# Kernel tuning notes

Measured on AMD Instinct MI355X. Metric: run time of the kernel, lower is better.

Reference implementation:

```python
import jax, jax.numpy as jnp
import numpy as np


def dct_matrix(n):
    # orthonormal DCT-II matrix, matches scipy.fftpack.dct(norm='ortho')
    k = jnp.arange(n, dtype=jnp.float32)[:, None]
    i = jnp.arange(n, dtype=jnp.float32)[None, :]
    D = jnp.cos(jnp.pi * (2.0 * i + 1.0) * k / (2.0 * n))
    s = jnp.where(k == 0, jnp.sqrt(1.0 / n), jnp.sqrt(2.0 / n))
    return (D * s).astype(jnp.float32)


def mad_mask(h, w):
    eps = 1e-10
    v1 = int(min(h, w) * 0.1)
    v2 = int(min(h, w) * 0.7)
    v3 = min(h, w)
    xy = jnp.maximum(jnp.arange(h, dtype=jnp.float32)[:, None],
                     jnp.arange(w, dtype=jnp.float32)[None, :])
    m = jnp.where(xy <= v1, 1.0 - xy / (v1 + eps) * 0.95,
        jnp.where(xy <= v2, 0.01,
        jnp.where(xy <= v3, (xy - v2) / (v3 - v2) * 0.3, 0.5)))
    return m.astype(jnp.float32)


def setup_inputs() -> dict:
    key = jax.random.key(0)
    ks = jax.random.split(key, 8)
    num_layers, token_length, C = 24, 100, 1024
    N, B = 1024, 32  # h = w = 32
    patch = 16
    val = np.sqrt(6.0 / float(3 * patch * patch + C))
    feats = jax.random.normal(ks[0], (1 + N, B, C), dtype=jnp.float32)
    learnable_tokens = jax.random.uniform(ks[1], (num_layers, token_length, C),
                                          minval=-val, maxval=val, dtype=jnp.float32)
    lim = 1.0 / np.sqrt(C)
    W_t2f = jax.random.uniform(ks[2], (C, C), minval=-lim, maxval=lim, dtype=jnp.float32)
    b_t2f = jax.random.uniform(ks[3], (C,), minval=-lim, maxval=lim, dtype=jnp.float32)
    W_df = jax.random.uniform(ks[4], (C, C), minval=-lim, maxval=lim, dtype=jnp.float32)
    b_df = jax.random.uniform(ks[5], (C,), minval=-lim, maxval=lim, dtype=jnp.float32)
    return {
        'feats': feats,
        'layer': 5,
        'learnable_tokens': learnable_tokens,
        'scale': jnp.float32(0.001),
        'W_t2f': W_t2f,
        'b_t2f': b_t2f,
        'W_df': W_df,
        'b_df': b_df,
    }


def reference(feats, layer, learnable_tokens, scale, W_t2f, b_t2f, W_df, b_df):
    # has_cls_token=True, batch_first=False (defaults)
    cls_tok, x = feats[:1], feats[1:]          # [1,B,C], [N,B,C]
    N, B, C = x.shape
    h = int(np.sqrt(N)); w = h
    # NOTE: original does a raw reshape (N,B,C) -> (B,C,h,w); replicate faithfully.
    ximg = x.reshape(B, C, h, w)
    # --- MAD_decompose: 2D orthonormal DCT-II per (b, c) image ---
    D = dct_matrix(h)
    feat_dct = jnp.einsum('ik,bckl,jl->bcij', D, ximg, D)
    mask = mad_mask(h, w)                      # [h,w]
    cal = feat_dct * (1.0 - mask)              # high-frequency (causal) part
    cal = cal.reshape(N, B, C)                 # raw reshape as in torch code
    # --- forward_delta_feat ---
    tokens = learnable_tokens[layer]           # [M,C]
    attn = jnp.einsum('nbc,mc->nbm', cal, tokens) * (C ** -0.5)
    attn = jax.nn.softmax(attn, axis=-1)
    t2f = tokens[1:] @ W_t2f.T + b_t2f         # [M-1,C]
    df = jnp.einsum('nbm,mc->nbc', attn[:, :, 1:], t2f)
    df = (df + cal) @ W_df.T + b_df            # [N,B,C]
    # --- MAD_compose_fast: ifft2 approximation of IDCT, clamp to [0,255] ---
    fc = df.reshape(B, C, h, w).astype(jnp.complex64)
    out = jnp.clip(jnp.real(jnp.fft.ifft2(fc, norm='ortho')), 0.0, 255.0)
    out = out.reshape(N, B, C).astype(jnp.float32)
    x = x + out * scale
    return jnp.concatenate([cls_tok, x], axis=0)
```

## Files before the change

kernel.cpp:

```cpp
#include <hip/hip_runtime.h>

typedef unsigned short u16;
typedef u16 ushort8 __attribute__((ext_vector_type(8)));
typedef u16 ushort4v __attribute__((ext_vector_type(4)));
typedef __bf16 bf16x8 __attribute__((ext_vector_type(8)));
typedef float f32x4 __attribute__((ext_vector_type(4)));

#define PI_F 3.14159265358979323846f

__device__ __forceinline__ u16 f2bf(float f) {
  union { float f; unsigned int u; } v; v.f = f;
  unsigned int r = v.u + 0x7fffu + ((v.u >> 16) & 1u);
  return (u16)(r >> 16);
}
__device__ __forceinline__ float bf2f(u16 u) {
  union { unsigned int u; float f; } v; v.u = ((unsigned int)u) << 16;
  return v.f;
}

__device__ __forceinline__ void gload16(const u16* g, u16* l) {
  __builtin_amdgcn_global_load_lds((const __attribute__((address_space(1))) void*)g,
                                   (__attribute__((address_space(3))) void*)l, 16, 0, 0);
}

__device__ __forceinline__ void stage_tile(const u16* __restrict__ G, int ld, int row0, int k0,
                                           u16* lds, int wid, int lane) {
  int seg = wid * 32;
  const u16* gp = G + (size_t)(row0 + seg + (lane >> 2)) * ld + k0 + (lane & 3) * 8;
  gload16(gp, lds + seg * 32);
  gload16(gp + (size_t)16 * ld, lds + (seg + 16) * 32);
}

#define WAIT_VM(N) asm volatile("s_waitcnt vmcnt(" #N ")" ::: "memory")
#define RAW_BARRIER() asm volatile("s_barrier" ::: "memory")

__device__ __forceinline__ float im_val(int r, int c) {
  float xy = (float)(r > c ? r : c);
  float m = (xy <= 3.0f) ? (1.0f - xy * (0.95f / 3.0f))
           : ((xy <= 22.0f) ? 0.01f : ((xy - 22.0f) * 0.03f));
  return 1.0f - m;
}
__device__ __forceinline__ float dct_val(int r, int c) {
  int a = ((2 * c + 1) * r) & 127;
  float s = (r == 0) ? 0.17677669529663687f : 0.25f;
  return cosf((float)a * (PI_F / 64.0f)) * s;
}

__device__ void mdct_row(const float* __restrict__ row, u16* __restrict__ dst, float* sm, int t) {
  float* Ms = sm; float* T1 = sm + 1056; float* Dsh = sm + 2112;
  for (int i = t; i < 1024; i += 256) {
    int r = i >> 5, c = i & 31;
    Dsh[r * 33 + c] = dct_val(r, c);
    Ms[r * 33 + c] = row[i] * im_val(r, c);
  }
  __syncthreads();
  int k = t >> 3, l0 = (t & 7) * 4;
  float a0 = 0, a1 = 0, a2 = 0, a3 = 0;
  #pragma unroll 8
  for (int i = 0; i < 32; ++i) {
    float d = Dsh[i * 33 + k];
    const float* mr = &Ms[i * 33 + l0];
    a0 += d * mr[0]; a1 += d * mr[1]; a2 += d * mr[2]; a3 += d * mr[3];
  }
  T1[k * 33 + l0 + 0] = a0; T1[k * 33 + l0 + 1] = a1;
  T1[k * 33 + l0 + 2] = a2; T1[k * 33 + l0 + 3] = a3;
  __syncthreads();
  float b0 = 0, b1 = 0, b2 = 0, b3 = 0;
  #pragma unroll 8
  for (int j = 0; j < 32; ++j) {
    float u = T1[k * 33 + j];
    b0 += u * Dsh[j * 33 + l0 + 0];
    b1 += u * Dsh[j * 33 + l0 + 1];
    b2 += u * Dsh[j * 33 + l0 + 2];
    b3 += u * Dsh[j * 33 + l0 + 3];
  }
  ushort4v o;
  o[0] = f2bf(b0); o[1] = f2bf(b1); o[2] = f2bf(b2); o[3] = f2bf(b3);
  *(ushort4v*)(dst + k * 32 + l0) = o;
}

__global__ __launch_bounds__(256) void k_stage1(const float* __restrict__ feats,
                                                const float* __restrict__ lt, const int* __restrict__ layerp,
                                                const float* __restrict__ Wt2f,
                                                const float* __restrict__ Wdf, const float* __restrict__ bdf,
                                                u16* __restrict__ xb, u16* __restrict__ wt_bf,
                                                u16* __restrict__ tok_bf, u16* __restrict__ A2,
                                                float* __restrict__ outp,
                                                float* __restrict__ weff_f, u16* __restrict__ weff_bf,
                                                float* __restrict__ beff, u16* __restrict__ tok2) {
  __shared__ __align__(16) float sm[14784];
  int bid = blockIdx.x, t = threadIdx.x;
  if (bid < 2048) {
    int tid = bid * 256 + t;
    int L = *layerp;
    const float4* in4 = (const float4*)(feats + 32768);
    ushort4v* xb4 = (ushort4v*)xb;
    #pragma unroll
    for (int rep = 0; rep < 16; ++rep) {
      int j = tid + rep * 524288;
      float4 v = in4[j];
      ushort4v o;
      o[0] = f2bf(v.x); o[1] = f2bf(v.y); o[2] = f2bf(v.z); o[3] = f2bf(v.w);
      xb4[j] = o;
    }
    ((ushort8*)A2)[tid] = (ushort8){0,0,0,0,0,0,0,0};
    if (tid < 262144) {
      float4 v = ((const float4*)Wt2f)[tid];
      ushort4v o;
      o[0] = f2bf(v.x); o[1] = f2bf(v.y); o[2] = f2bf(v.z); o[3] = f2bf(v.w);
      ((ushort4v*)wt_bf)[tid] = o;
    }
    if (tid < 32768) {
      outp[tid] = feats[tid];
      int m = tid >> 8;
      ushort4v o = (ushort4v){0,0,0,0};
      if (m < 99) {
        float4 v = *(const float4*)(lt + (size_t)L * 102400 + (size_t)(m + 1) * 1024 + (tid & 255) * 4);
        o[0] = f2bf(v.x); o[1] = f2bf(v.y); o[2] = f2bf(v.z); o[3] = f2bf(v.w);
      }
      ((ushort4v*)tok_bf)[tid] = o;
    }
    return;
  }
  int b2 = bid - 2048;
  if (b2 < 256) {
    float* In = sm; float* Uc = sm + 4224; float* Us = sm + 8448;
    float* Csh = sm + 12672; float* Ssh = sm + 13728;
    int c0 = b2 * 4;
    for (int i = t; i < 1024; i += 256) {
      int r = i >> 5, c = i & 31;
      float ang = (float)((r * c) & 31) * (PI_F / 16.0f);
      Csh[r * 33 + c] = cosf(ang); Ssh[r * 33 + c] = sinf(ang);
    }
    { int cc = t & 3, v0 = t >> 2;
      for (int v = v0; v < 1024; v += 64)
        In[cc * 1056 + (v >> 5) * 33 + (v & 31)] = Wdf[(size_t)v * 1024 + c0 + cc]; }
    __syncthreads();
    int cc = t >> 6, L2 = t & 63, p = L2 & 31, h = L2 >> 5;
    for (int j = h * 16; j < h * 16 + 16; ++j) {
      float ac = 0, as = 0;
      #pragma unroll 8
      for (int i = 0; i < 32; ++i) {
        float m = In[cc * 1056 + i * 33 + j];
        ac += Csh[p * 33 + i] * m;
        as += Ssh[p * 33 + i] * m;
      }
      Uc[cc * 1056 + p * 33 + j] = ac;
      Us[cc * 1056 + p * 33 + j] = as;
    }
    __syncthreads();
    for (int q = h * 16; q < h * 16 + 16; ++q) {
      float acc = 0;
      #pragma unroll 8
      for (int j = 0; j < 32; ++j)
        acc += Uc[cc * 1056 + p * 33 + j] * Csh[q * 33 + j] -
               Us[cc * 1056 + p * 33 + j] * Ssh[q * 33 + j];
      float val = acc * 0.03125f;
      size_t idx = (size_t)(p * 32 + q) * 1024 + c0 + cc;
      weff_f[idx] = val;
      weff_bf[idx] = f2bf(val);
    }
  } else if (b2 == 256) {
    float* Bsh = sm; float* Uc = sm + 1056; float* Us = sm + 2112;
    float* Csh = sm + 3168; float* Ssh = sm + 4224;
    for (int i = t; i < 1024; i += 256) {
      int r = i >> 5, c = i & 31;
      float ang = (float)((r * c) & 31) * (PI_F / 16.0f);
      Csh[r * 33 + c] = cosf(ang); Ssh[r * 33 + c] = sinf(ang);
      Bsh[r * 33 + c] = bdf[i];
    }
    __syncthreads();
    for (int idx = t; idx < 1024; idx += 256) {
      int p = idx >> 5, j = idx & 31;
      float ac = 0, as = 0;
      #pragma unroll 8
      for (int i = 0; i < 32; ++i) {
        float m = Bsh[i * 33 + j];
        ac += Csh[p * 33 + i] * m;
        as += Ssh[p * 33 + i] * m;
      }
      Uc[p * 33 + j] = ac; Us[p * 33 + j] = as;
    }
    __syncthreads();
    for (int idx = t; idx < 1024; idx += 256) {
      int p = idx >> 5, q = idx & 31;
      float acc = 0;
      #pragma unroll 8
      for (int jj = 0; jj < 32; ++jj)
        acc += Uc[p * 33 + jj] * Csh[q * 33 + jj] - Us[p * 33 + jj] * Ssh[q * 33 + jj];
      beff[idx] = acc * 0.03125f;
    }
  } else {
    int p = b2 - 257;
    if (p >= 100) {
      *(ushort4v*)(tok2 + (size_t)p * 1024 + t * 4) = (ushort4v){0,0,0,0};
      return;
    }
    mdct_row(lt + (size_t)(*layerp) * 102400 + (size_t)p * 1024, tok2 + (size_t)p * 1024, sm, t);
  }
}

template <int NT>
__device__ __forceinline__ void gemm128_core(const u16* __restrict__ A, int lda,
                                             const u16* __restrict__ B, int ldb,
                                             int g0, int c0, u16* smem,
                                             f32x4 (&acc)[4][4], int wid, int lane) {
  int wr = wid >> 1, wc = wid & 1, cl = lane & 15, rg = lane >> 4;
  stage_tile(A, lda, g0, 0, smem, wid, lane);
  stage_tile(B, ldb, c0, 0, smem + 12288, wid, lane);
  stage_tile(A, lda, g0, 32, smem + 4096, wid, lane);
  stage_tile(B, ldb, c0, 32, smem + 16384, wid, lane);
  int cur = 0;
  #pragma unroll 1
  for (int kt = 0; kt < NT; ++kt) {
    if (kt == NT - 1) { WAIT_VM(0); } else { WAIT_VM(4); }
    RAW_BARRIER();
    if (kt + 2 < NT) {
      int slot = (cur == 0) ? 2 : cur - 1;
      stage_tile(A, lda, g0, (kt + 2) * 32, smem + slot * 4096, wid, lane);
      stage_tile(B, ldb, c0, (kt + 2) * 32, smem + 12288 + slot * 4096, wid, lane);
    }
    const u16* pa = smem + cur * 4096;
    const u16* pb = smem + 12288 + cur * 4096;
    bf16x8 af[4], bv[4];
    #pragma unroll
    for (int mf = 0; mf < 4; mf++)
      af[mf] = *(const bf16x8*)(pa + (wr * 64 + mf * 16 + cl) * 32 + rg * 8);
    #pragma unroll
    for (int nf = 0; nf < 4; nf++)
      bv[nf] = *(const bf16x8*)(pb + (wc * 64 + nf * 16 + cl) * 32 + rg * 8);
    #pragma unroll
    for (int mf = 0; mf < 4; mf++)
      #pragma unroll
      for (int nf = 0; nf < 4; nf++)
        acc[mf][nf] = __builtin_amdgcn_mfma_f32_16x16x32_bf16(af[mf], bv[nf], acc[mf][nf], 0, 0, 0);
    cur = (cur == 2) ? 0 : cur + 1;
  }
}

__global__ __launch_bounds__(256) void k_stage2(const float* __restrict__ weff_f,
                                                const u16* __restrict__ tok_bf, const u16* __restrict__ wt_bf,
                                                const float* __restrict__ bt2f,
                                                const u16* __restrict__ xb, const u16* __restrict__ tok2,
                                                u16* __restrict__ w2, u16* __restrict__ t2f,
                                                u16* __restrict__ A2) {
  __shared__ __align__(16) u16 smem[24576];
  int bid = blockIdx.x, t = threadIdx.x;
  int lane = t & 63, wid = t >> 6;
  if (bid < 1024) {
    mdct_row(weff_f + (size_t)bid * 1024, w2 + (size_t)bid * 1024, (float*)smem, t);
  } else if (bid < 1032) {
    int bn = bid - 1024;
    int wr = wid >> 1, wc = wid & 1, cl = lane & 15, rg = lane >> 4;
    f32x4 acc[4][4];
    #pragma unroll
    for (int i = 0; i < 4; i++)
      #pragma unroll
      for (int j = 0; j < 4; j++) acc[i][j] = (f32x4){0.f,0.f,0.f,0.f};
    gemm128_core<32>(tok_bf, 1024, wt_bf, 1024, 0, bn * 128, smem, acc, wid, lane);
    #pragma unroll
    for (int mf = 0; mf < 4; mf++)
      #pragma unroll
      for (int nf = 0; nf < 4; nf++) {
        int col = bn * 128 + wc * 64 + nf * 16 + cl;
        #pragma unroll
        for (int r = 0; r < 4; r++) {
          int row = wr * 64 + mf * 16 + rg * 4 + r;
          t2f[(size_t)row * 1024 + col] = (row < 99) ? f2bf(acc[mf][nf][r] + bt2f[col]) : (u16)0;
        }
      }
  } else {
    int g0 = (bid - 1032) * 128;
    int cl = lane & 15, rg = lane >> 4;
    f32x4 acc[2][7];
    #pragma unroll
    for (int i = 0; i < 2; i++)
      #pragma unroll
      for (int j = 0; j < 7; j++) acc[i][j] = (f32x4){0.f,0.f,0.f,0.f};
    stage_tile(xb, 1024, g0, 0, smem, wid, lane);
    stage_tile(tok2, 1024, 0, 0, smem + 12288, wid, lane);
    stage_tile(xb, 1024, g0, 32, smem + 4096, wid, lane);
    stage_tile(tok2, 1024, 0, 32, smem + 16384, wid, lane);
    int cur = 0;
    #pragma unroll 1
    for (int kt = 0; kt < 32; ++kt) {
      if (kt == 31) { WAIT_VM(0); } else { WAIT_VM(4); }
      RAW_BARRIER();
      if (kt + 2 < 32) {
        int slot = (cur == 0) ? 2 : cur - 1;
        stage_tile(xb, 1024, g0, (kt + 2) * 32, smem + slot * 4096, wid, lane);
        stage_tile(tok2, 1024, 0, (kt + 2) * 32, smem + 12288 + slot * 4096, wid, lane);
      }
      const u16* pa = smem + cur * 4096;
      const u16* pb = smem + 12288 + cur * 4096;
      bf16x8 a0 = *(const bf16x8*)(pa + (wid * 32 + cl) * 32 + rg * 8);
      bf16x8 a1 = *(const bf16x8*)(pa + (wid * 32 + 16 + cl) * 32 + rg * 8);
      #pragma unroll
      for (int nf = 0; nf < 7; nf++) {
        bf16x8 bv = *(const bf16x8*)(pb + (nf * 16 + cl) * 32 + rg * 8);
        acc[0][nf] = __builtin_amdgcn_mfma_f32_16x16x32_bf16(a0, bv, acc[0][nf], 0, 0, 0);
        acc[1][nf] = __builtin_amdgcn_mfma_f32_16x16x32_bf16(a1, bv, acc[1][nf], 0, 0, 0);
      }
      cur = (cur == 2) ? 0 : cur + 1;
    }
    #pragma unroll
    for (int mf = 0; mf < 2; mf++) {
      #pragma unroll
      for (int r = 0; r < 4; r++) {
        int grow = g0 + wid * 32 + mf * 16 + rg * 4 + r;
        float v[7];
        float mx = -1e30f;
        #pragma unroll
        for (int nf = 0; nf < 7; nf++) {
          int m = nf * 16 + cl;
          v[nf] = acc[mf][nf][r] * 0.03125f;
          if (m < 100) mx = fmaxf(mx, v[nf]);
        }
        #pragma unroll
        for (int d = 1; d < 16; d <<= 1) mx = fmaxf(mx, __shfl_xor(mx, d));
        float s = 0;
        #pragma unroll
        for (int nf = 0; nf < 7; nf++) {
          int m = nf * 16 + cl;
          float e = (m < 100) ? __expf(v[nf] - mx) : 0.0f;
          v[nf] = e; s += e;
        }
        #pragma unroll
        for (int d = 1; d < 16; d <<= 1) s += __shfl_xor(s, d);
        float inv = 1.0f / s;
        #pragma unroll
        for (int nf = 0; nf < 7; nf++) {
          int m = nf * 16 + cl;
          if (m >= 1 && m < 100) A2[(size_t)grow * 128 + (m - 1)] = f2bf(v[nf] * inv);
        }
      }
    }
  }
}

__global__ __launch_bounds__(256) void k_gt(const u16* __restrict__ weff_bf, const u16* __restrict__ t2f,
                                            u16* __restrict__ Gt) {
  __shared__ __align__(16) u16 smem[24576];
  int bid = blockIdx.x, t = threadIdx.x;
  int lane = t & 63, wid = t >> 6;
  int wr = wid >> 1, wc = wid & 1, cl = lane & 15, rg = lane >> 4;
  f32x4 acc[4][4];
  #pragma unroll
  for (int i = 0; i < 4; i++)
    #pragma unroll
    for (int j = 0; j < 4; j++) acc[i][j] = (f32x4){0.f,0.f,0.f,0.f};
  gemm128_core<32>(weff_bf, 1024, t2f, 1024, bid * 128, 0, smem, acc, wid, lane);
  #pragma unroll
  for (int mf = 0; mf < 4; mf++)
    #pragma unroll
    for (int nf = 0; nf < 4; nf++) {
      int col = wc * 64 + nf * 16 + cl;
      #pragma unroll
      for (int r = 0; r < 4; r++) {
        int row = bid * 128 + wr * 64 + mf * 16 + rg * 4 + r;
        Gt[(size_t)row * 128 + col] = f2bf(acc[mf][nf][r]);
      }
    }
}

__global__ __launch_bounds__(512, 2) void k_main(const u16* __restrict__ xb, const u16* __restrict__ w2,
                                                 const u16* __restrict__ a2, const u16* __restrict__ gt,
                                                 const float* __restrict__ beff, const float* __restrict__ feats,
                                                 const float* __restrict__ scalep, float* __restrict__ outf) {
  __shared__ __align__(16) u16 smem[49152];
  int tid = threadIdx.x, lane = tid & 63, wid = tid >> 6;
  int wr = wid >> 2, wc = wid & 3;
  int cl = lane & 15, rg = lane >> 4;
  int bid = blockIdx.x;
  int swz = (bid & 7) * 64 + (bid >> 3);
  int bm = swz >> 2, bn = swz & 3;
  int g0 = bm * 256, c0 = bn * 256;

  f32x4 acc[8][4];
  #pragma unroll
  for (int i = 0; i < 8; i++)
    #pragma unroll
    for (int j = 0; j < 4; j++) acc[i][j] = (f32x4){0.f,0.f,0.f,0.f};

  const int NT = 36;

  int offA[8], offB[4];
  #pragma unroll
  for (int mf = 0; mf < 8; ++mf) {
    int r = wr * 128 + mf * 16 + cl;
    int lrow = r >> 1;
    offA[mf] = lrow * 64 + (((((r & 1) << 2) | rg) ^ (lrow & 7)) << 3);
  }
  #pragma unroll
  for (int nf = 0; nf < 4; ++nf) {
    int r = wc * 64 + nf * 16 + cl;
    int lrow = r >> 1;
    offB[nf] = lrow * 64 + (((((r & 1) << 2) | rg) ^ (lrow & 7)) << 3);
  }

  auto issueA = [&](int t) {
    u16* R = smem + (t % 3) * 8192;
    const u16* G = (t < 32) ? xb : a2;
    int ld = (t < 32) ? 1024 : 128;
    int k0 = (t < 32) ? t * 32 : (t - 32) * 32;
    #pragma unroll
    for (int p = 0; p < 2; ++p) {
      int lrow = p * 64 + wid * 8 + (lane >> 3);
      int c2 = (lane & 7) ^ (lrow & 7);
      const u16* src = G + (size_t)(g0 + 2 * lrow + (c2 >> 2)) * ld + k0 + (c2 & 3) * 8;
      gload16(src, R + (p * 64 + wid * 8) * 64);
    }
  };
  auto issueB = [&](int t) {
    u16* R = smem + 24576 + (t % 3) * 8192;
    const u16* G = (t < 32) ? w2 : gt;
    int ld = (t < 32) ? 1024 : 128;
    int k0 = (t < 32) ? t * 32 : (t - 32) * 32;
    #pragma unroll
    for (int p = 0; p < 2; ++p) {
      int lrow = p * 64 + wid * 8 + (lane >> 3);
      int c2 = (lane & 7) ^ (lrow & 7);
      const u16* src = G + (size_t)(c0 + 2 * lrow + (c2 >> 2)) * ld + k0 + (c2 & 3) * 8;
      gload16(src, R + (p * 64 + wid * 8) * 64);
    }
  };

  issueA(0); issueB(0);
  issueA(1); issueB(1);

  #pragma unroll 1
  for (int t = 0; t < NT; ++t) {
    if (t == NT - 1) { WAIT_VM(0); } else { WAIT_VM(4); }
    RAW_BARRIER();
    int slot = t % 3;
    const u16* pa = smem + slot * 8192;
    const u16* pb = smem + 24576 + slot * 8192;
    bf16x8 af[8], bv[4];
    #pragma unroll
    for (int nf = 0; nf < 4; ++nf) bv[nf] = *(const bf16x8*)(pb + offB[nf]);
    #pragma unroll
    for (int mf = 0; mf < 8; ++mf) af[mf] = *(const bf16x8*)(pa + offA[mf]);
    if (t + 2 < NT) { issueA(t + 2); issueB(t + 2); }
    __builtin_amdgcn_s_setprio(1);
    #pragma unroll
    for (int mf = 0; mf < 8; ++mf)
      #pragma unroll
      for (int nf = 0; nf < 4; ++nf)
        acc[mf][nf] = __builtin_amdgcn_mfma_f32_16x16x32_bf16(af[mf], bv[nf], acc[mf][nf], 0, 0, 0);
    __builtin_amdgcn_s_setprio(0);
  }

  float sc = *scalep;
  #pragma unroll
  for (int mf = 0; mf < 8; mf++) {
    #pragma unroll
    for (int nf = 0; nf < 4; nf++) {
      int col = c0 + wc * 64 + nf * 16 + cl;
      #pragma unroll
      for (int r = 0; r < 4; r++) {
        int row = g0 + wr * 128 + mf * 16 + rg * 4 + r;
        size_t idx = (size_t)row * 1024 + col;
        float val = acc[mf][nf][r] + beff[col];
        float rr = fminf(fmaxf(val, 0.f), 255.f);
        outf[32768 + idx] = feats[32768 + idx] + rr * sc;
      }
    }
  }
}

extern "C" void kernel_launch(void* const* d_in, const int* in_sizes, int n_in,
                              void* d_out, int out_size, void* d_ws, size_t ws_size,
                              hipStream_t stream) {
  const float* feats  = (const float*)d_in[0];
  const int*   layerp = (const int*)d_in[1];
  const float* lt     = (const float*)d_in[2];
  const float* scalep = (const float*)d_in[3];
  const float* Wt2f   = (const float*)d_in[4];
  const float* bt2f   = (const float*)d_in[5];
  const float* Wdf    = (const float*)d_in[6];
  const float* bdf    = (const float*)d_in[7];
  float* outp = (float*)d_out;

  char* ws = (char*)d_ws;
  float* beff   = (float*)(ws + 0);
  float* weff_f = (float*)(ws + 65536);
  u16* weff_bf = (u16*)(ws + 4259840);
  u16* w2      = (u16*)(ws + 6356992);
  u16* tok_bf  = (u16*)(ws + 8454144);
  u16* wt_bf   = (u16*)(ws + 8716288);
  u16* tok2    = (u16*)(ws + 10813440);
  u16* t2f     = (u16*)(ws + 11075584);
  u16* Gt      = (u16*)(ws + 11337728);
  u16* A2      = (u16*)(ws + 11599872);
  u16* xb      = (u16*)(ws + 19988480);

  k_stage1<<<2433, 256, 0, stream>>>(feats, lt, layerp, Wt2f, Wdf, bdf,
                                     xb, wt_bf, tok_bf, A2, outp, weff_f, weff_bf, beff, tok2);
  k_stage2<<<1288, 256, 0, stream>>>(weff_f, tok_bf, wt_bf, bt2f, xb, tok2, w2, t2f, A2);
  k_gt<<<8, 256, 0, stream>>>(weff_bf, t2f, Gt);
  k_main<<<512, 512, 0, stream>>>(xb, w2, A2, Gt, beff, feats, scalep, outp);
}
```

Measured before the change: 232.8 us.

## Compute t2f in stage1, fold Gt GEMM into stage2, double-buffer main

The token-to-feature projection now runs in fp32 inside stage1 as 128 extra blocks using a scalar dot-product loop, so the bf16 conversion of W_t2f and the tokens is dropped. The Gt GEMM moves into stage2, which removes the separate k_gt launch. k_main's pipeline goes from three shared-memory buffers with prefetch distance two to two buffers with distance one, cutting LDS use to allow higher occupancy. The trade-off is less load/compute overlap in the main GEMM, plus a slow scalar matvec that each block runs over the whole 4 MB weight matrix.

```diff
diff --git a/kernel.cpp b/kernel.cpp
--- a/kernel.cpp
+++ b/kernel.cpp
@@ -81,18 +81,17 @@
 
 __global__ __launch_bounds__(256) void k_stage1(const float* __restrict__ feats,
                                                 const float* __restrict__ lt, const int* __restrict__ layerp,
-                                                const float* __restrict__ Wt2f,
+                                                const float* __restrict__ Wt2f, const float* __restrict__ bt2f,
                                                 const float* __restrict__ Wdf, const float* __restrict__ bdf,
-                                                u16* __restrict__ xb, u16* __restrict__ wt_bf,
-                                                u16* __restrict__ tok_bf, u16* __restrict__ A2,
+                                                u16* __restrict__ xb, u16* __restrict__ A2,
                                                 float* __restrict__ outp,
                                                 float* __restrict__ weff_f, u16* __restrict__ weff_bf,
-                                                float* __restrict__ beff, u16* __restrict__ tok2) {
+                                                float* __restrict__ beff, u16* __restrict__ tok2,
+                                                u16* __restrict__ t2f) {
   __shared__ __align__(16) float sm[14784];
   int bid = blockIdx.x, t = threadIdx.x;
   if (bid < 2048) {
     int tid = bid * 256 + t;
-    int L = *layerp;
     const float4* in4 = (const float4*)(feats + 32768);
     ushort4v* xb4 = (ushort4v*)xb;
     #pragma unroll
@@ -104,22 +103,7 @@
       xb4[j] = o;
     }
     ((ushort8*)A2)[tid] = (ushort8){0,0,0,0,0,0,0,0};
-    if (tid < 262144) {
-      float4 v = ((const float4*)Wt2f)[tid];
-      ushort4v o;
-      o[0] = f2bf(v.x); o[1] = f2bf(v.y); o[2] = f2bf(v.z); o[3] = f2bf(v.w);
-      ((ushort4v*)wt_bf)[tid] = o;
-    }
-    if (tid < 32768) {
-      outp[tid] = feats[tid];
-      int m = tid >> 8;
-      ushort4v o = (ushort4v){0,0,0,0};
-      if (m < 99) {
-        float4 v = *(const float4*)(lt + (size_t)L * 102400 + (size_t)(m + 1) * 1024 + (tid & 255) * 4);
-        o[0] = f2bf(v.x); o[1] = f2bf(v.y); o[2] = f2bf(v.z); o[3] = f2bf(v.w);
-      }
-      ((ushort4v*)tok_bf)[tid] = o;
-    }
+    if (tid < 32768) outp[tid] = feats[tid];
     return;
   }
   int b2 = bid - 2048;
@@ -190,13 +174,35 @@
         acc += Uc[p * 33 + jj] * Csh[q * 33 + jj] - Us[p * 33 + jj] * Ssh[q * 33 + jj];
       beff[idx] = acc * 0.03125f;
     }
-  } else {
+  } else if (b2 < 385) {
     int p = b2 - 257;
     if (p >= 100) {
       *(ushort4v*)(tok2 + (size_t)p * 1024 + t * 4) = (ushort4v){0,0,0,0};
       return;
     }
     mdct_row(lt + (size_t)(*layerp) * 102400 + (size_t)p * 1024, tok2 + (size_t)p * 1024, sm, t);
+  } else {
+    int m = b2 - 385;
+    if (m >= 99) {
+      for (int c = t; c < 1024; c += 256) t2f[(size_t)m * 1024 + c] = 0;
+      return;
+    }
+    float* tokrow = sm;
+    int L = *layerp;
+    const float* tr = lt + (size_t)L * 102400 + (size_t)(m + 1) * 1024;
+    for (int i = t; i < 1024; i += 256) tokrow[i] = tr[i];
+    __syncthreads();
+    for (int c = t; c < 1024; c += 256) {
+      const float4* w4 = (const float4*)(Wt2f + (size_t)c * 1024);
+      float acc = 0;
+      #pragma unroll 4
+      for (int k = 0; k < 256; k++) {
+        float4 w = w4[k];
+        acc += tokrow[4 * k + 0] * w.x + tokrow[4 * k + 1] * w.y +
+               tokrow[4 * k + 2] * w.z + tokrow[4 * k + 3] * w.w;
+      }
+      t2f[(size_t)m * 1024 + c] = f2bf(acc + bt2f[c]);
+    }
   }
 }
 
@@ -239,38 +245,34 @@
 }
 
 __global__ __launch_bounds__(256) void k_stage2(const float* __restrict__ weff_f,
-                                                const u16* __restrict__ tok_bf, const u16* __restrict__ wt_bf,
-                                                const float* __restrict__ bt2f,
+                                                const u16* __restrict__ weff_bf, const u16* __restrict__ t2f,
                                                 const u16* __restrict__ xb, const u16* __restrict__ tok2,
-                                                u16* __restrict__ w2, u16* __restrict__ t2f,
+                                                u16* __restrict__ w2, u16* __restrict__ Gt,
                                                 u16* __restrict__ A2) {
   __shared__ __align__(16) u16 smem[24576];
   int bid = blockIdx.x, t = threadIdx.x;
   int lane = t & 63, wid = t >> 6;
-  if (bid < 1024) {
-    mdct_row(weff_f + (size_t)bid * 1024, w2 + (size_t)bid * 1024, (float*)smem, t);
-  } else if (bid < 1032) {
-    int bn = bid - 1024;
+  if (bid < 8) {
     int wr = wid >> 1, wc = wid & 1, cl = lane & 15, rg = lane >> 4;
     f32x4 acc[4][4];
     #pragma unroll
     for (int i = 0; i < 4; i++)
       #pragma unroll
       for (int j = 0; j < 4; j++) acc[i][j] = (f32x4){0.f,0.f,0.f,0.f};
-    gemm128_core<32>(tok_bf, 1024, wt_bf, 1024, 0, bn * 128, smem, acc, wid, lane);
+    gemm128_core<32>(weff_bf, 1024, t2f, 1024, bid * 128, 0, smem, acc, wid, lane);
     #pragma unroll
     for (int mf = 0; mf < 4; mf++)
       #pragma unroll
       for (int nf = 0; nf < 4; nf++) {
-        int col = bn * 128 + wc * 64 + nf * 16 + cl;
+        int col = wc * 64 + nf * 16 + cl;
         #pragma unroll
         for (int r = 0; r < 4; r++) {
-          int row = wr * 64 + mf * 16 + rg * 4 + r;
-          t2f[(size_t)row * 1024 + col] = (row < 99) ? f2bf(acc[mf][nf][r] + bt2f[col]) : (u16)0;
+          int row = bid * 128 + wr * 64 + mf * 16 + rg * 4 + r;
+          Gt[(size_t)row * 128 + col] = f2bf(acc[mf][nf][r]);
         }
       }
-  } else {
-    int g0 = (bid - 1032) * 128;
+  } else if (bid < 264) {
+    int g0 = (bid - 8) * 128;
     int cl = lane & 15, rg = lane >> 4;
     f32x4 acc[2][7];
     #pragma unroll
@@ -335,39 +337,16 @@
         }
       }
     }
-  }
-}
-
-__global__ __launch_bounds__(256) void k_gt(const u16* __restrict__ weff_bf, const u16* __restrict__ t2f,
-                                            u16* __restrict__ Gt) {
-  __shared__ __align__(16) u16 smem[24576];
-  int bid = blockIdx.x, t = threadIdx.x;
-  int lane = t & 63, wid = t >> 6;
-  int wr = wid >> 1, wc = wid & 1, cl = lane & 15, rg = lane >> 4;
-  f32x4 acc[4][4];
-  #pragma unroll
-  for (int i = 0; i < 4; i++)
-    #pragma unroll
-    for (int j = 0; j < 4; j++) acc[i][j] = (f32x4){0.f,0.f,0.f,0.f};
-  gemm128_core<32>(weff_bf, 1024, t2f, 1024, bid * 128, 0, smem, acc, wid, lane);
-  #pragma unroll
-  for (int mf = 0; mf < 4; mf++)
-    #pragma unroll
-    for (int nf = 0; nf < 4; nf++) {
-      int col = wc * 64 + nf * 16 + cl;
-      #pragma unroll
-      for (int r = 0; r < 4; r++) {
-        int row = bid * 128 + wr * 64 + mf * 16 + rg * 4 + r;
-        Gt[(size_t)row * 128 + col] = f2bf(acc[mf][nf][r]);
-      }
-    }
+  } else {
+    mdct_row(weff_f + (size_t)(bid - 264) * 1024, w2 + (size_t)(bid - 264) * 1024, (float*)smem, t);
+  }
 }
 
 __global__ __launch_bounds__(512, 2) void k_main(const u16* __restrict__ xb, const u16* __restrict__ w2,
                                                  const u16* __restrict__ a2, const u16* __restrict__ gt,
                                                  const float* __restrict__ beff, const float* __restrict__ feats,
                                                  const float* __restrict__ scalep, float* __restrict__ outf) {
-  __shared__ __align__(16) u16 smem[49152];
+  __shared__ __align__(16) u16 smem[32768];
   int tid = threadIdx.x, lane = tid & 63, wid = tid >> 6;
   int wr = wid >> 2, wc = wid & 3;
   int cl = lane & 15, rg = lane >> 4;
@@ -399,7 +378,7 @@
   }
 
   auto issueA = [&](int t) {
-    u16* R = smem + (t % 3) * 8192;
+    u16* R = smem + (t & 1) * 8192;
     const u16* G = (t < 32) ? xb : a2;
     int ld = (t < 32) ? 1024 : 128;
     int k0 = (t < 32) ? t * 32 : (t - 32) * 32;
@@ -412,7 +391,7 @@
     }
   };
   auto issueB = [&](int t) {
-    u16* R = smem + 24576 + (t % 3) * 8192;
+    u16* R = smem + 16384 + (t & 1) * 8192;
     const u16* G = (t < 32) ? w2 : gt;
     int ld = (t < 32) ? 1024 : 128;
     int k0 = (t < 32) ? t * 32 : (t - 32) * 32;
@@ -426,21 +405,20 @@
   };
 
   issueA(0); issueB(0);
-  issueA(1); issueB(1);
 
   #pragma unroll 1
   for (int t = 0; t < NT; ++t) {
-    if (t == NT - 1) { WAIT_VM(0); } else { WAIT_VM(4); }
+    WAIT_VM(0);
     RAW_BARRIER();
-    int slot = t % 3;
+    if (t + 1 < NT) { issueA(t + 1); issueB(t + 1); }
+    int slot = t & 1;
     const u16* pa = smem + slot * 8192;
-    const u16* pb = smem + 24576 + slot * 8192;
+    const u16* pb = smem + 16384 + slot * 8192;
     bf16x8 af[8], bv[4];
     #pragma unroll
     for (int nf = 0; nf < 4; ++nf) bv[nf] = *(const bf16x8*)(pb + offB[nf]);
     #pragma unroll
     for (int mf = 0; mf < 8; ++mf) af[mf] = *(const bf16x8*)(pa + offA[mf]);
-    if (t + 2 < NT) { issueA(t + 2); issueB(t + 2); }
     __builtin_amdgcn_s_setprio(1);
     #pragma unroll
     for (int mf = 0; mf < 8; ++mf)
@@ -486,17 +464,14 @@
   float* weff_f = (float*)(ws + 65536);
   u16* weff_bf = (u16*)(ws + 4259840);
   u16* w2      = (u16*)(ws + 6356992);
-  u16* tok_bf  = (u16*)(ws + 8454144);
-  u16* wt_bf   = (u16*)(ws + 8716288);
   u16* tok2    = (u16*)(ws + 10813440);
   u16* t2f     = (u16*)(ws + 11075584);
   u16* Gt      = (u16*)(ws + 11337728);
   u16* A2      = (u16*)(ws + 11599872);
   u16* xb      = (u16*)(ws + 19988480);
 
-  k_stage1<<<2433, 256, 0, stream>>>(feats, lt, layerp, Wt2f, Wdf, bdf,
-                                     xb, wt_bf, tok_bf, A2, outp, weff_f, weff_bf, beff, tok2);
-  k_stage2<<<1288, 256, 0, stream>>>(weff_f, tok_bf, wt_bf, bt2f, xb, tok2, w2, t2f, A2);
-  k_gt<<<8, 256, 0, stream>>>(weff_bf, t2f, Gt);
+  k_stage1<<<2561, 256, 0, stream>>>(feats, lt, layerp, Wt2f, bt2f, Wdf, bdf,
+                                     xb, A2, outp, weff_f, weff_bf, beff, tok2, t2f);
+  k_stage2<<<1288, 256, 0, stream>>>(weff_f, weff_bf, t2f, xb, tok2, w2, Gt, A2);
   k_main<<<512, 512, 0, stream>>>(xb, w2, A2, Gt, beff, feats, scalep, outp);
 }
```

Result: slower. 397.6 us (+70.8%).
